# Optimization experiments

Measured on AMD Instinct MI355X. Metric: run time of the kernel, lower is better.

Reference implementation:

```python
import jax, jax.numpy as jnp
import numpy as np

B, S, D = 4, 2048, 768
H, E = 12, 64  # num_heads, head_size


def setup_inputs() -> dict:
    key = jax.random.key(0)
    ks = jax.random.split(key, 9)
    sd = 1.0 / np.sqrt(D)
    return {
        "x": jax.random.normal(ks[0], (B, S, D), dtype=jnp.float32),
        "Wq": jax.random.normal(ks[1], (H, D, E), dtype=jnp.float32) * sd,
        "bq": jax.random.normal(ks[2], (H, E), dtype=jnp.float32) * 0.02,
        "Wk": jax.random.normal(ks[3], (H, D, E), dtype=jnp.float32) * sd,
        "bk": jax.random.normal(ks[4], (H, E), dtype=jnp.float32) * 0.02,
        "Wv": jax.random.normal(ks[5], (H, D, E), dtype=jnp.float32) * sd,
        "bv": jax.random.normal(ks[6], (H, E), dtype=jnp.float32) * 0.02,
        "Wp": jax.random.normal(ks[7], (H * E, D), dtype=jnp.float32) * sd,
        "bp": jax.random.normal(ks[8], (D,), dtype=jnp.float32) * 0.02,
    }


def reference(x, Wq, bq, Wk, bk, Wv, bv, Wp, bp):
    # Batched multi-head QKV projections (replaces per-head Python loop)
    q = jnp.einsum("bsd,hde->bhse", x, Wq) + bq[None, :, None, :]
    k = jnp.einsum("bsd,hde->bhse", x, Wk) + bk[None, :, None, :]
    v = jnp.einsum("bsd,hde->bhse", x, Wv) + bv[None, :, None, :]
    scale = 1.0 / jnp.sqrt(jnp.asarray(E, dtype=x.dtype))
    # Full materialized attention matrix [B,H,S,S] as in the original module
    wei = jnp.einsum("bhqe,bhke->bhqk", q, k) * scale
    wei = jax.nn.softmax(wei, axis=-1)  # dropout=0 (eval) => identity
    out = jnp.einsum("bhqk,bhke->bhqe", wei, v)  # [B,H,S,E]
    # concat heads in head order then output projection
    out = out.transpose(0, 2, 1, 3).reshape(B, S, H * E)
    return out @ Wp + bp
```

## Files before the change

### kernel.cpp

```cpp
#include <hip/hip_runtime.h>
#include <cstddef>
#include <cstdint>

#define NB 4
#define NH 12
#define SQ 2048
#define DM 768
#define EH 64
#define MTOT (NB*SQ)
#define NQKV (NH*3*EH)

typedef __attribute__((ext_vector_type(8))) short short8;
typedef __attribute__((ext_vector_type(4))) float floatx4;

#define QSCALE 0.18033688011112042f

__device__ __forceinline__ unsigned short f2bf(float f) {
    unsigned int u = __float_as_uint(f);
    u += 0x7fffu + ((u >> 16) & 1u);
    return (unsigned short)(u >> 16);
}

#if __has_builtin(__builtin_amdgcn_exp2f)
__device__ __forceinline__ float fast_exp2(float x) { return __builtin_amdgcn_exp2f(x); }
#else
__device__ __forceinline__ float fast_exp2(float x) { return exp2f(x); }
#endif

#if __has_builtin(__builtin_amdgcn_cvt_pk_bf16_f32)
typedef __attribute__((ext_vector_type(2))) __bf16 bf16x2_t;
__device__ __forceinline__ unsigned int pack_bf16(float lo, float hi) {
    bf16x2_t v = __builtin_amdgcn_cvt_pk_bf16_f32(lo, hi);
    return __builtin_bit_cast(unsigned int, v);
}
#else
__device__ __forceinline__ unsigned int pack_bf16(float lo, float hi) {
    unsigned int u0 = __float_as_uint(lo) + 0x8000u;
    unsigned int u1 = __float_as_uint(hi) + 0x8000u;
    return __builtin_amdgcn_perm(u1, u0, 0x07060302u);
}
#endif
__device__ __forceinline__ short8 pack8(float a0,float a1,float a2,float a3,
                                        float b0,float b1,float b2,float b3) {
    union { unsigned int u[4]; short8 s; } cv;
    cv.u[0] = pack_bf16(a0, a1);
    cv.u[1] = pack_bf16(a2, a3);
    cv.u[2] = pack_bf16(b0, b1);
    cv.u[3] = pack_bf16(b2, b3);
    return cv.s;
}
__device__ __forceinline__ void gl_lds16(const void* g, void* l) {
    __builtin_amdgcn_global_load_lds(
        (const __attribute__((address_space(1))) unsigned int*)g,
        (__attribute__((address_space(3))) unsigned int*)l, 16, 0, 0);
}

#define CVT_A 1572864
#define CVT_B (CVT_A + 442368)
#define CVT_C (CVT_B + 147456)
#define CVT_D (CVT_C + 576)
__global__ __launch_bounds__(256) void convert_pack(
    const float* __restrict__ x,
    const float* __restrict__ Wq, const float* __restrict__ bq,
    const float* __restrict__ Wk, const float* __restrict__ bk,
    const float* __restrict__ Wv, const float* __restrict__ bv,
    const float* __restrict__ Wp,
    unsigned short* __restrict__ Xb, unsigned short* __restrict__ Wt,
    unsigned short* __restrict__ Wpt, float* __restrict__ bias_all)
{
    int t = blockIdx.x * 256 + threadIdx.x;
    if (t < CVT_A) {
        float4 v = ((const float4*)x)[t];
        ushort4 r; r.x = f2bf(v.x); r.y = f2bf(v.y); r.z = f2bf(v.z); r.w = f2bf(v.w);
        ((ushort4*)Xb)[t] = r;
    } else if (t < CVT_B) {
        int u = t - CVT_A;
        int n = u / 192, kc = (u % 192) * 4;
        int h = n / 192, rr = n % 192, wsel = rr >> 6, e = rr & 63;
        const float* W = (wsel == 0) ? Wq : ((wsel == 1) ? Wk : Wv);
        float sc = (wsel == 0) ? QSCALE : 1.0f;
        ushort4 r;
        r.x = f2bf(W[((size_t)h * DM + kc + 0) * EH + e] * sc);
        r.y = f2bf(W[((size_t)h * DM + kc + 1) * EH + e] * sc);
        r.z = f2bf(W[((size_t)h * DM + kc + 2) * EH + e] * sc);
        r.w = f2bf(W[((size_t)h * DM + kc + 3) * EH + e] * sc);
        ((ushort4*)Wt)[u] = r;
    } else if (t < CVT_C) {
        int u = t - CVT_B;
        int n = u / 192, kc = (u % 192) * 4;
        ushort4 r;
        r.x = f2bf(Wp[(size_t)(kc + 0) * DM + n]);
        r.y = f2bf(Wp[(size_t)(kc + 1) * DM + n]);
        r.z = f2bf(Wp[(size_t)(kc + 2) * DM + n]);
        r.w = f2bf(Wp[(size_t)(kc + 3) * DM + n]);
        ((ushort4*)Wpt)[u] = r;
    } else if (t < CVT_D) {
        int u = (t - CVT_C) * 4;
        #pragma unroll
        for (int j = 0; j < 4; j++) {
            int n = u + j;
            int h = n / 192, rr = n % 192, wsel = rr >> 6, e = rr & 63;
            const float* bs = (wsel == 0) ? bq : ((wsel == 1) ? bk : bv);
            bias_all[n] = bs[h * EH + e] * ((wsel == 0) ? QSCALE : 1.0f);
        }
    }
}

__global__ __launch_bounds__(256) void qkv_mfma(
    const unsigned short* __restrict__ Xb, const unsigned short* __restrict__ Wt,
    const float* __restrict__ bias_all,
    unsigned short* __restrict__ Qo, unsigned short* __restrict__ Kf,
    unsigned short* __restrict__ Vf)
{
    __shared__ unsigned short As[2][128 * 32];
    __shared__ unsigned short Bs[2][128 * 32];
    __shared__ unsigned short Ep[4][16 * 72];
    const int tid = threadIdx.x;
    const int w = tid >> 6, lane = tid & 63;
    const int l15 = lane & 15, quad = lane >> 4;
    const int wm = w & 1, wn = w >> 1;
    const int m0 = blockIdx.x * 128, n0 = blockIdx.y * 128;
    const int srow = w * 32 + (lane >> 2);
    const int pchunk = lane & 3;

    floatx4 acc[4][4];
    #pragma unroll
    for (int i = 0; i < 4; i++)
        #pragma unroll
        for (int j = 0; j < 4; j++) acc[i][j] = 0;

    #pragma unroll
    for (int c = 0; c < 2; c++) {
        int mr = srow + c * 16;
        int j = (pchunk - (mr >> 1)) & 3;
        gl_lds16(&Xb[(size_t)(m0 + mr) * DM + j * 8],
                 &As[0][w * 1024 + c * 512 + lane * 8]);
        gl_lds16(&Wt[(size_t)(n0 + mr) * DM + j * 8],
                 &Bs[0][w * 1024 + c * 512 + lane * 8]);
    }

    for (int kt = 0; kt < DM / 32; kt++) {
        const int cur = kt & 1;
        __syncthreads();
        if (kt + 1 < DM / 32) {
            int k0n = (kt + 1) * 32;
            #pragma unroll
            for (int c = 0; c < 2; c++) {
                int mr = srow + c * 16;
                int j = (pchunk - (mr >> 1)) & 3;
                gl_lds16(&Xb[(size_t)(m0 + mr) * DM + k0n + j * 8],
                         &As[cur ^ 1][w * 1024 + c * 512 + lane * 8]);
                gl_lds16(&Wt[(size_t)(n0 + mr) * DM + k0n + j * 8],
                         &Bs[cur ^ 1][w * 1024 + c * 512 + lane * 8]);
            }
        }
        short8 af[4], bf[4];
        #pragma unroll
        for (int mi = 0; mi < 4; mi++) {
            int row = wm * 64 + mi * 16 + l15;
            int pp = (quad + (row >> 1)) & 3;
            af[mi] = *(const short8*)&As[cur][row * 32 + pp * 8];
        }
        #pragma unroll
        for (int ni = 0; ni < 4; ni++) {
            int row = wn * 64 + ni * 16 + l15;
            int pp = (quad + (row >> 1)) & 3;
            bf[ni] = *(const short8*)&Bs[cur][row * 32 + pp * 8];
        }
        #pragma unroll
        for (int mi = 0; mi < 4; mi++)
            #pragma unroll
            for (int ni = 0; ni < 4; ni++)
                acc[mi][ni] = __builtin_amdgcn_mfma_f32_16x16x32_bf16(
                    af[mi], bf[ni], acc[mi][ni], 0, 0, 0);
    }
    __syncthreads();

    const int bB = m0 >> 11;
    const int ntb0 = n0 + wn * 64;
    const int h = ntb0 / 192, rr = ntb0 % 192;
    const int wsel = rr >> 6;
    const size_t bhbase = ((size_t)bB * NH + h) * (SQ * EH);
    const int sb_base = (m0 & 2047) + wm * 64;
    unsigned short* Ew = &Ep[w][0];
    float bvv[4];
    #pragma unroll
    for (int ni = 0; ni < 4; ni++) bvv[ni] = bias_all[ntb0 + ni * 16 + l15];

    if (wsel == 0) {
        #pragma unroll
        for (int mi = 0; mi < 4; mi++) {
            #pragma unroll
            for (int ni = 0; ni < 4; ni++)
                #pragma unroll
                for (int r = 0; r < 4; r++)
                    Ew[(quad * 4 + r) * 72 + ni * 16 + l15] =
                        f2bf(acc[mi][ni][r] + bvv[ni]);
            #pragma unroll
            for (int t = 0; t < 2; t++) {
                uint4 d = *(uint4*)&Ew[(t * 8 + (lane >> 3)) * 72 + (lane & 7) * 8];
                *(uint4*)&Qo[bhbase +
                    (size_t)(sb_base + mi * 16 + t * 8 + (lane >> 3)) * EH +
                    (lane & 7) * 8] = d;
            }
        }
    } else if (wsel == 1) {
        size_t tbase = bhbase + (size_t)(sb_base >> 6) * 4096;
        #pragma unroll
        for (int mi = 0; mi < 4; mi++) {
            #pragma unroll
            for (int ni = 0; ni < 4; ni++)
                #pragma unroll
                for (int r = 0; r < 4; r++)
                    Ew[(quad * 4 + r) * 72 + ni * 16 + l15] =
                        f2bf(acc[mi][ni][r] + bvv[ni]);
            #pragma unroll
            for (int t = 0; t < 2; t++) {
                uint4 d = *(uint4*)&Ew[l15 * 72 + t * 32 + quad * 8];
                *(uint4*)&Kf[tbase +
                    (size_t)((mi * 2 + t) * 64 + quad * 16 + l15) * 8] = d;
            }
        }
    } else {
        size_t tbase = bhbase + (size_t)(sb_base >> 6) * 4096;
        #pragma unroll
        for (int ni = 0; ni < 4; ni++) {
            #pragma unroll
            for (int mi = 0; mi < 4; mi++)
                #pragma unroll
                for (int r = 0; r < 4; r += 2) {
                    unsigned int pr = pack_bf16(acc[mi][ni][r]     + bvv[ni],
                                                acc[mi][ni][r + 1] + bvv[ni]);
                    *(unsigned int*)&Ew[l15 * 72 + quad * 16 + mi * 4 + r] = pr;
                }
            #pragma unroll
            for (int t = 0; t < 2; t++) {
                uint4 d = *(uint4*)&Ew[l15 * 72 + t * 32 + quad * 8];
                int unit = (ni * 2 + (quad & 1)) * 64 + ((quad >> 1) + 2 * t) * 16 + l15;
                *(uint4*)&Vf[tbase + (size_t)unit * 8] = d;
            }
        }
    }
}

__global__ __launch_bounds__(256, 2) void attn_mfma(
    const unsigned short* __restrict__ Q, const unsigned short* __restrict__ Kf,
    const unsigned short* __restrict__ Vf, unsigned short* __restrict__ O)
{
    __shared__ unsigned short Ks[4][4096];
    __shared__ unsigned short Vs[4][4096];
    const int tid = threadIdx.x;
    const int w = tid >> 6, lane = tid & 63;
    const int l15 = lane & 15, quad = lane >> 4;
    const int wq = w & 1;
    const int wk = w >> 1;
    const int bh = blockIdx.x;
    const int b = bh / NH, h = bh % NH;
    const int q0 = blockIdx.y * 128;

    const unsigned short* Qb = Q + (size_t)bh * SQ * EH;
    const unsigned short* Kb = Kf + (size_t)bh * SQ * EH;
    const unsigned short* Vb = Vf + (size_t)bh * SQ * EH;

    short8 qf[4][2];
    #pragma unroll
    for (int qh = 0; qh < 4; qh++)
        #pragma unroll
        for (int kh = 0; kh < 2; kh++)
            qf[qh][kh] = *(const short8*)
                &Qb[(size_t)(q0 + wq * 64 + qh * 16 + l15) * EH + kh * 32 + quad * 8];

    short8 ones;
    #pragma unroll
    for (int j = 0; j < 8; j++) ones[j] = (short)0x3F80;
    const floatx4 fzero = 0;

    floatx4 o[4][4], l_acc[4];
    #pragma unroll
    for (int qh = 0; qh < 4; qh++) {
        l_acc[qh] = 0;
        #pragma unroll
        for (int nb = 0; nb < 4; nb++) o[qh][nb] = 0;
    }

    #pragma unroll
    for (int c = 0; c < 4; c++) {
        int sg = wq * 4 + c;
        gl_lds16(&Kb[(size_t)wk * 4096 + sg * 512 + lane * 8],
                 &Ks[wk][sg * 512 + lane * 8]);
        gl_lds16(&Vb[(size_t)wk * 4096 + sg * 512 + lane * 8],
                 &Vs[wk][sg * 512 + lane * 8]);
    }
    asm volatile("s_waitcnt vmcnt(0)\n\ts_barrier" ::: "memory");

    for (int j = 0; j < SQ / 128; j++) {
        const int tj = 2 * j + wk;
        const int bc = tj & 3;
        if (j + 1 < SQ / 128) {
            const int tn = tj + 2, bn = bc ^ 2;
            #pragma unroll
            for (int c = 0; c < 4; c++) {
                int sg = wq * 4 + c;
                gl_lds16(&Kb[(size_t)tn * 4096 + sg * 512 + lane * 8],
                         &Ks[bn][sg * 512 + lane * 8]);
                gl_lds16(&Vb[(size_t)tn * 4096 + sg * 512 + lane * 8],
                         &Vs[bn][sg * 512 + lane * 8]);
            }
        }
        short8 kf[4][2], vf[4][2];
        #pragma unroll
        for (int nb = 0; nb < 4; nb++)
            #pragma unroll
            for (int kh = 0; kh < 2; kh++)
                kf[nb][kh] = *(const short8*)&Ks[bc][((nb * 2 + kh) * 64 + lane) * 8];
        #pragma unroll
        for (int eb = 0; eb < 4; eb++)
            #pragma unroll
            for (int kh = 0; kh < 2; kh++)
                vf[eb][kh] = *(const short8*)&Vs[bc][((eb * 2 + kh) * 64 + lane) * 8];

        #pragma unroll
        for (int qh = 0; qh < 4; qh++) {
            floatx4 s[4];
            __builtin_amdgcn_s_setprio(1);
            #pragma unroll
            for (int nb = 0; nb < 4; nb++) {
                floatx4 z = __builtin_amdgcn_mfma_f32_16x16x32_bf16(
                    kf[nb][0], qf[qh][0], fzero, 0, 0, 0);
                s[nb] = __builtin_amdgcn_mfma_f32_16x16x32_bf16(
                    kf[nb][1], qf[qh][1], z, 0, 0, 0);
            }
            __builtin_amdgcn_s_setprio(0);
            float p[4][4];
            #pragma unroll
            for (int nb = 0; nb < 4; nb++)
                #pragma unroll
                for (int r = 0; r < 4; r++)
                    p[nb][r] = fast_exp2(s[nb][r]);
            short8 pa0 = pack8(p[0][0], p[0][1], p[0][2], p[0][3],
                               p[1][0], p[1][1], p[1][2], p[1][3]);
            short8 pa1 = pack8(p[2][0], p[2][1], p[2][2], p[2][3],
                               p[3][0], p[3][1], p[3][2], p[3][3]);
            __builtin_amdgcn_s_setprio(1);
            l_acc[qh] = __builtin_amdgcn_mfma_f32_16x16x32_bf16(pa0, ones, l_acc[qh], 0, 0, 0);
            l_acc[qh] = __builtin_amdgcn_mfma_f32_16x16x32_bf16(pa1, ones, l_acc[qh], 0, 0, 0);
            #pragma unroll
            for (int eb = 0; eb < 4; eb++) {
                o[qh][eb] = __builtin_amdgcn_mfma_f32_16x16x32_bf16(pa0, vf[eb][0], o[qh][eb], 0, 0, 0);
                o[qh][eb] = __builtin_amdgcn_mfma_f32_16x16x32_bf16(pa1, vf[eb][1], o[qh][eb], 0, 0, 0);
            }
            __builtin_amdgcn_s_setprio(0);
        }
        if (j + 1 < SQ / 128)
            asm volatile("s_waitcnt vmcnt(0)\n\ts_barrier" ::: "memory");
    }

    __syncthreads();
    float* Xo = (float*)&Ks[0][0];
    float* Xl = (float*)&Vs[0][0];
    if (wk == 1) {
        float* po = Xo + wq * 4096;
        float* pl = Xl + wq * 1024;
        #pragma unroll
        for (int qh = 0; qh < 4; qh++) {
            #pragma unroll
            for (int eb = 0; eb < 4; eb++)
                *(floatx4*)&po[((qh * 4 + eb) * 64 + lane) * 4] = o[qh][eb];
            *(floatx4*)&pl[(qh * 64 + lane) * 4] = l_acc[qh];
        }
    }
    __syncthreads();
    if (wk == 0) {
        float* po = Xo + wq * 4096;
        float* pl = Xl + wq * 1024;
        #pragma unroll
        for (int qh = 0; qh < 4; qh++) {
            #pragma unroll
            for (int eb = 0; eb < 4; eb++)
                o[qh][eb] += *(floatx4*)&po[((qh * 4 + eb) * 64 + lane) * 4];
            l_acc[qh] += *(floatx4*)&pl[(qh * 64 + lane) * 4];
        }
        #pragma unroll
        for (int qh = 0; qh < 4; qh++)
            #pragma unroll
            for (int r = 0; r < 4; r++) {
                float inv = 1.0f / l_acc[qh][r];
                int sidx = q0 + wq * 64 + qh * 16 + quad * 4 + r;
                size_t base = (((size_t)b * SQ + sidx) * NH + h) * EH + l15;
                O[base +  0] = f2bf(o[qh][0][r] * inv);
                O[base + 16] = f2bf(o[qh][1][r] * inv);
                O[base + 32] = f2bf(o[qh][2][r] * inv);
                O[base + 48] = f2bf(o[qh][3][r] * inv);
            }
    }
}

__global__ __launch_bounds__(256) void proj_mfma(
    const unsigned short* __restrict__ Ab, const unsigned short* __restrict__ Wpt,
    const float* __restrict__ bp, float* __restrict__ C)
{
    __shared__ unsigned short As[2][64 * 32];
    __shared__ unsigned short Bs[2][128 * 32];
    __shared__ float Epf[4][16 * 68];
    const int tid = threadIdx.x;
    const int w = tid >> 6, lane = tid & 63;
    const int l15 = lane & 15, quad = lane >> 4;
    const int wm = w & 1, wn = w >> 1;
    const int m0 = blockIdx.x * 64, n0 = blockIdx.y * 128;
    const int pchunk = lane & 3;

    floatx4 acc[2][4];
    #pragma unroll
    for (int i = 0; i < 2; i++)
        #pragma unroll
        for (int j = 0; j < 4; j++) acc[i][j] = 0;

    {
        int mr = w * 16 + (lane >> 2);
        int j = (pchunk - (mr >> 1)) & 3;
        gl_lds16(&Ab[(size_t)(m0 + mr) * DM + j * 8], &As[0][w * 512 + lane * 8]);
    }
    #pragma unroll
    for (int c = 0; c < 2; c++) {
        int nr = w * 32 + c * 16 + (lane >> 2);
        int j = (pchunk - (nr >> 1)) & 3;
        gl_lds16(&Wpt[(size_t)(n0 + nr) * DM + j * 8],
                 &Bs[0][w * 1024 + c * 512 + lane * 8]);
    }

    for (int kt = 0; kt < DM / 32; kt++) {
        const int cur = kt & 1;
        __syncthreads();
        if (kt + 1 < DM / 32) {
            int k0n = (kt + 1) * 32;
            {
                int mr = w * 16 + (lane >> 2);
                int j = (pchunk - (mr >> 1)) & 3;
                gl_lds16(&Ab[(size_t)(m0 + mr) * DM + k0n + j * 8],
                         &As[cur ^ 1][w * 512 + lane * 8]);
            }
            #pragma unroll
            for (int c = 0; c < 2; c++) {
                int nr = w * 32 + c * 16 + (lane >> 2);
                int j = (pchunk - (nr >> 1)) & 3;
                gl_lds16(&Wpt[(size_t)(n0 + nr) * DM + k0n + j * 8],
                         &Bs[cur ^ 1][w * 1024 + c * 512 + lane * 8]);
            }
        }
        short8 af[2], bf[4];
        #pragma unroll
        for (int mi = 0; mi < 2; mi++) {
            int row = wm * 32 + mi * 16 + l15;
            int pp = (quad + (row >> 1)) & 3;
            af[mi] = *(const short8*)&As[cur][row * 32 + pp * 8];
        }
        #pragma unroll
        for (int ni = 0; ni < 4; ni++) {
            int row = wn * 64 + ni * 16 + l15;
            int pp = (quad + (row >> 1)) & 3;
            bf[ni] = *(const short8*)&Bs[cur][row * 32 + pp * 8];
        }
        #pragma unroll
        for (int mi = 0; mi < 2; mi++)
            #pragma unroll
            for (int ni = 0; ni < 4; ni++)
                acc[mi][ni] = __builtin_amdgcn_mfma_f32_16x16x32_bf16(
                    af[mi], bf[ni], acc[mi][ni], 0, 0, 0);
    }
    __syncthreads();

    float* Ewf = &Epf[w][0];
    float bvv[4];
    #pragma unroll
    for (int ni = 0; ni < 4; ni++) bvv[ni] = bp[n0 + wn * 64 + ni * 16 + l15];
    #pragma unroll
    for (int mi = 0; mi < 2; mi++) {
        #pragma unroll
        for (int ni = 0; ni < 4; ni++)
            #pragma unroll
            for (int r = 0; r < 4; r++)
                Ewf[(quad * 4 + r) * 68 + ni * 16 + l15] = acc[mi][ni][r] + bvv[ni];
        #pragma unroll
        for (int t = 0; t < 4; t++) {
            float4 d = *(float4*)&Ewf[(t * 4 + quad) * 68 + l15 * 4];
            *(float4*)&C[(size_t)(m0 + wm * 32 + mi * 16 + t * 4 + quad) * DM +
                         n0 + wn * 64 + l15 * 4] = d;
        }
    }
}

extern "C" void kernel_launch(void* const* d_in, const int* in_sizes, int n_in,
                              void* d_out, int out_size, void* d_ws, size_t ws_size,
                              hipStream_t stream) {
    const float* x  = (const float*)d_in[0];
    const float* Wq = (const float*)d_in[1];
    const float* bq = (const float*)d_in[2];
    const float* Wk = (const float*)d_in[3];
    const float* bk = (const float*)d_in[4];
    const float* Wv = (const float*)d_in[5];
    const float* bv = (const float*)d_in[6];
    const float* Wp = (const float*)d_in[7];
    const float* bp = (const float*)d_in[8];
    float* out = (float*)d_out;

    const size_t QKV_ELEMS = (size_t)NB * NH * SQ * EH;
    unsigned short* Qb   = (unsigned short*)d_ws;
    unsigned short* Kfb  = Qb + QKV_ELEMS;
    unsigned short* Vfb  = Kfb + QKV_ELEMS;
    unsigned short* Abuf = Vfb + QKV_ELEMS;
    unsigned short* Xb   = Abuf + QKV_ELEMS;
    unsigned short* Wtb  = Xb + QKV_ELEMS;
    unsigned short* Wptb = Wtb + (size_t)NQKV * DM;
    float* bias_all      = (float*)(Wptb + (size_t)DM * DM);

    convert_pack<<<(CVT_D + 255) / 256, 256, 0, stream>>>(
        x, Wq, bq, Wk, bk, Wv, bv, Wp, Xb, Wtb, Wptb, bias_all);
    qkv_mfma<<<dim3(MTOT / 128, NQKV / 128), 256, 0, stream>>>(
        Xb, Wtb, bias_all, Qb, Kfb, Vfb);
    attn_mfma<<<dim3(NB * NH, SQ / 128), 256, 0, stream>>>(Qb, Kfb, Vfb, Abuf);
    proj_mfma<<<dim3(MTOT / 64, DM / 128), 256, 0, stream>>>(Abuf, Wptb, bp, out);
}
```

Baseline: 236.9 us.

## Split each K/V tile across wave pairs with triple-buffered LDS pipeline

```diff
diff --git a/kernel.cpp b/kernel.cpp
--- a/kernel.cpp
+++ b/kernel.cpp
@@ -243,17 +243,17 @@
     }
 }
 
-__global__ __launch_bounds__(256, 2) void attn_mfma(
+__global__ __launch_bounds__(256, 3) void attn_mfma(
     const unsigned short* __restrict__ Q, const unsigned short* __restrict__ Kf,
     const unsigned short* __restrict__ Vf, unsigned short* __restrict__ O)
 {
-    __shared__ unsigned short Ks[4][4096];
-    __shared__ unsigned short Vs[4][4096];
+    __shared__ __align__(16) unsigned short Ks[3 * 4096];
+    __shared__ __align__(16) unsigned short Vs[3 * 4096];
     const int tid = threadIdx.x;
     const int w = tid >> 6, lane = tid & 63;
     const int l15 = lane & 15, quad = lane >> 4;
     const int wq = w & 1;
-    const int wk = w >> 1;
+    const int wp = w >> 1;
     const int bh = blockIdx.x;
     const int b = bh / NH, h = bh % NH;
     const int q0 = blockIdx.y * 128;
@@ -280,105 +280,100 @@
     for (int qh = 0; qh < 4; qh++) {
         l_acc[qh] = 0;
         #pragma unroll
-        for (int nb = 0; nb < 4; nb++) o[qh][nb] = 0;
-    }
-
-    #pragma unroll
-    for (int c = 0; c < 4; c++) {
-        int sg = wq * 4 + c;
-        gl_lds16(&Kb[(size_t)wk * 4096 + sg * 512 + lane * 8],
-                 &Ks[wk][sg * 512 + lane * 8]);
-        gl_lds16(&Vb[(size_t)wk * 4096 + sg * 512 + lane * 8],
-                 &Vs[wk][sg * 512 + lane * 8]);
+        for (int eb = 0; eb < 4; eb++) o[qh][eb] = 0;
+    }
+
+    const int seg = w * 2;
+    #pragma unroll
+    for (int c = 0; c < 2; c++) {
+        gl_lds16(&Kb[(seg + c) * 512 + lane * 8], &Ks[(seg + c) * 512 + lane * 8]);
+        gl_lds16(&Vb[(seg + c) * 512 + lane * 8], &Vs[(seg + c) * 512 + lane * 8]);
+    }
+    #pragma unroll
+    for (int c = 0; c < 2; c++) {
+        gl_lds16(&Kb[4096 + (seg + c) * 512 + lane * 8],
+                 &Ks[4096 + (seg + c) * 512 + lane * 8]);
+        gl_lds16(&Vb[4096 + (seg + c) * 512 + lane * 8],
+                 &Vs[4096 + (seg + c) * 512 + lane * 8]);
     }
     asm volatile("s_waitcnt vmcnt(0)\n\ts_barrier" ::: "memory");
 
-    for (int j = 0; j < SQ / 128; j++) {
-        const int tj = 2 * j + wk;
-        const int bc = tj & 3;
-        if (j + 1 < SQ / 128) {
-            const int tn = tj + 2, bn = bc ^ 2;
-            #pragma unroll
-            for (int c = 0; c < 4; c++) {
-                int sg = wq * 4 + c;
-                gl_lds16(&Kb[(size_t)tn * 4096 + sg * 512 + lane * 8],
-                         &Ks[bn][sg * 512 + lane * 8]);
-                gl_lds16(&Vb[(size_t)tn * 4096 + sg * 512 + lane * 8],
-                         &Vs[bn][sg * 512 + lane * 8]);
-            }
-        }
-        short8 kf[4][2], vf[4][2];
-        #pragma unroll
-        for (int nb = 0; nb < 4; nb++)
+    const int kblk = 4 * wp;
+    int offC = 0, offN = 4096, offS = 8192;
+    for (int t = 0; t < SQ / 64; t++) {
+        if (t + 2 < SQ / 64) {
+            const unsigned short* Kn = Kb + (size_t)(t + 2) * 4096;
+            const unsigned short* Vn = Vb + (size_t)(t + 2) * 4096;
+            #pragma unroll
+            for (int c = 0; c < 2; c++) {
+                gl_lds16(&Kn[(seg + c) * 512 + lane * 8],
+                         &Ks[offS + (seg + c) * 512 + lane * 8]);
+                gl_lds16(&Vn[(seg + c) * 512 + lane * 8],
+                         &Vs[offS + (seg + c) * 512 + lane * 8]);
+            }
+        }
+        short8 kf[2][2], vf[4];
+        #pragma unroll
+        for (int nb2 = 0; nb2 < 2; nb2++)
             #pragma unroll
             for (int kh = 0; kh < 2; kh++)
-                kf[nb][kh] = *(const short8*)&Ks[bc][((nb * 2 + kh) * 64 + lane) * 8];
+                kf[nb2][kh] = *(const short8*)
+                    &Ks[offC + ((kblk + nb2 * 2 + kh) * 64 + lane) * 8];
         #pragma unroll
         for (int eb = 0; eb < 4; eb++)
-            #pragma unroll
-            for (int kh = 0; kh < 2; kh++)
-                vf[eb][kh] = *(const short8*)&Vs[bc][((eb * 2 + kh) * 64 + lane) * 8];
+            vf[eb] = *(const short8*)&Vs[offC + ((eb * 2 + wp) * 64 + lane) * 8];
 
         #pragma unroll
         for (int qh = 0; qh < 4; qh++) {
-            floatx4 s[4];
             __builtin_amdgcn_s_setprio(1);
-            #pragma unroll
-            for (int nb = 0; nb < 4; nb++) {
-                floatx4 z = __builtin_amdgcn_mfma_f32_16x16x32_bf16(
-                    kf[nb][0], qf[qh][0], fzero, 0, 0, 0);
-                s[nb] = __builtin_amdgcn_mfma_f32_16x16x32_bf16(
-                    kf[nb][1], qf[qh][1], z, 0, 0, 0);
-            }
+            floatx4 s0 = __builtin_amdgcn_mfma_f32_16x16x32_bf16(
+                kf[0][0], qf[qh][0], fzero, 0, 0, 0);
+            s0 = __builtin_amdgcn_mfma_f32_16x16x32_bf16(
+                kf[0][1], qf[qh][1], s0, 0, 0, 0);
+            floatx4 s1 = __builtin_amdgcn_mfma_f32_16x16x32_bf16(
+                kf[1][0], qf[qh][0], fzero, 0, 0, 0);
+            s1 = __builtin_amdgcn_mfma_f32_16x16x32_bf16(
+                kf[1][1], qf[qh][1], s1, 0, 0, 0);
             __builtin_amdgcn_s_setprio(0);
-            float p[4][4];
-            #pragma unroll
-            for (int nb = 0; nb < 4; nb++)
-                #pragma unroll
-                for (int r = 0; r < 4; r++)
-                    p[nb][r] = fast_exp2(s[nb][r]);
-            short8 pa0 = pack8(p[0][0], p[0][1], p[0][2], p[0][3],
-                               p[1][0], p[1][1], p[1][2], p[1][3]);
-            short8 pa1 = pack8(p[2][0], p[2][1], p[2][2], p[2][3],
-                               p[3][0], p[3][1], p[3][2], p[3][3]);
+            float p0[4], p1[4];
+            #pragma unroll
+            for (int r = 0; r < 4; r++) {
+                p0[r] = fast_exp2(s0[r]);
+                p1[r] = fast_exp2(s1[r]);
+            }
+            short8 pa = pack8(p0[0], p0[1], p0[2], p0[3],
+                              p1[0], p1[1], p1[2], p1[3]);
             __builtin_amdgcn_s_setprio(1);
-            l_acc[qh] = __builtin_amdgcn_mfma_f32_16x16x32_bf16(pa0, ones, l_acc[qh], 0, 0, 0);
-            l_acc[qh] = __builtin_amdgcn_mfma_f32_16x16x32_bf16(pa1, ones, l_acc[qh], 0, 0, 0);
-            #pragma unroll
-            for (int eb = 0; eb < 4; eb++) {
-                o[qh][eb] = __builtin_amdgcn_mfma_f32_16x16x32_bf16(pa0, vf[eb][0], o[qh][eb], 0, 0, 0);
-                o[qh][eb] = __builtin_amdgcn_mfma_f32_16x16x32_bf16(pa1, vf[eb][1], o[qh][eb], 0, 0, 0);
-            }
+            l_acc[qh] = __builtin_amdgcn_mfma_f32_16x16x32_bf16(pa, ones, l_acc[qh], 0, 0, 0);
+            #pragma unroll
+            for (int eb = 0; eb < 4; eb++)
+                o[qh][eb] = __builtin_amdgcn_mfma_f32_16x16x32_bf16(pa, vf[eb], o[qh][eb], 0, 0, 0);
             __builtin_amdgcn_s_setprio(0);
         }
-        if (j + 1 < SQ / 128)
+        if (t + 1 < SQ / 64)
             asm volatile("s_waitcnt vmcnt(0)\n\ts_barrier" ::: "memory");
+        int tmp = offC; offC = offN; offN = offS; offS = tmp;
     }
 
     __syncthreads();
-    float* Xo = (float*)&Ks[0][0];
-    float* Xl = (float*)&Vs[0][0];
-    if (wk == 1) {
-        float* po = Xo + wq * 4096;
-        float* pl = Xl + wq * 1024;
+    float* base = wq ? (float*)Vs : (float*)Ks;
+    if (wp == 1) {
         #pragma unroll
         for (int qh = 0; qh < 4; qh++) {
             #pragma unroll
             for (int eb = 0; eb < 4; eb++)
-                *(floatx4*)&po[((qh * 4 + eb) * 64 + lane) * 4] = o[qh][eb];
-            *(floatx4*)&pl[(qh * 64 + lane) * 4] = l_acc[qh];
+                *(floatx4*)&base[((qh * 4 + eb) * 64 + lane) * 4] = o[qh][eb];
+            *(floatx4*)&base[4096 + (qh * 64 + lane) * 4] = l_acc[qh];
         }
     }
     __syncthreads();
-    if (wk == 0) {
-        float* po = Xo + wq * 4096;
-        float* pl = Xl + wq * 1024;
+    if (wp == 0) {
         #pragma unroll
         for (int qh = 0; qh < 4; qh++) {
             #pragma unroll
             for (int eb = 0; eb < 4; eb++)
-                o[qh][eb] += *(floatx4*)&po[((qh * 4 + eb) * 64 + lane) * 4];
-            l_acc[qh] += *(floatx4*)&pl[(qh * 64 + lane) * 4];
+                o[qh][eb] += *(floatx4*)&base[((qh * 4 + eb) * 64 + lane) * 4];
+            l_acc[qh] += *(floatx4*)&base[4096 + (qh * 64 + lane) * 4];
         }
         #pragma unroll
         for (int qh = 0; qh < 4; qh++)
@@ -386,11 +381,11 @@
             for (int r = 0; r < 4; r++) {
                 float inv = 1.0f / l_acc[qh][r];
                 int sidx = q0 + wq * 64 + qh * 16 + quad * 4 + r;
-                size_t base = (((size_t)b * SQ + sidx) * NH + h) * EH + l15;
-                O[base +  0] = f2bf(o[qh][0][r] * inv);
-                O[base + 16] = f2bf(o[qh][1][r] * inv);
-                O[base + 32] = f2bf(o[qh][2][r] * inv);
-                O[base + 48] = f2bf(o[qh][3][r] * inv);
+                size_t ob = (((size_t)b * SQ + sidx) * NH + h) * EH + l15;
+                O[ob +  0] = f2bf(o[qh][0][r] * inv);
+                O[ob + 16] = f2bf(o[qh][1][r] * inv);
+                O[ob + 32] = f2bf(o[qh][2][r] * inv);
+                O[ob + 48] = f2bf(o[qh][3][r] * inv);
             }
     }
 }
```

Result: no change. 235.8 us (-0.4%).
